# Optimization experiments

Hardware: AMD Instinct MI355X
Metric: run time of the kernel (lower is better)

## Reference

```python
import jax, jax.numpy as jnp
import numpy as np

NUM_HEADS = 8

def conv1x1(x, w, b):
    # x: [B,C,H,W], w: [O,C], b: [O]
    return jnp.einsum('bchw,oc->bohw', x, w) + b[None, :, None, None]

def setup_inputs() -> dict:
    key = jax.random.key(0)
    ks = jax.random.split(key, 8)
    B, C, H, W = 8, 256, 32, 32
    HF, WF = 128, 128
    s = 1.0 / np.sqrt(C)  # xavier-ish scale for 1x1 convs
    return {
        'x': jax.random.normal(ks[0], (B, C, H, W), jnp.float32),
        'featmap': jax.random.normal(ks[1], (B, C, HF, WF), jnp.float32),
        'wq': jax.random.normal(ks[2], (C, C), jnp.float32) * s,
        'bq': jnp.zeros((C,), jnp.float32),
        'wk': jax.random.normal(ks[3], (C, C), jnp.float32) * s,
        'bk': jnp.zeros((C,), jnp.float32),
        'wv': jax.random.normal(ks[4], (C, C), jnp.float32) * s,
        'bv': jnp.zeros((C,), jnp.float32),
        'wg': jax.random.normal(ks[5], (1, C), jnp.float32) * s,
        'bg': jnp.zeros((1,), jnp.float32),
    }

def _to_grid(t, h, w, rh, rw):
    # t: [B8, d, h*rh, w*rw] -> [B8, d, h, w, rh*rw] (aligned local grid per query pixel)
    b8, d = t.shape[:2]
    t = t.reshape(b8, d, h, rh, w, rw)
    return t.transpose(0, 1, 2, 4, 3, 5).reshape(b8, d, h, w, rh * rw)

def reference(x, featmap, wq, bq, wk, bk, wv, bv, wg, bg):
    B, C, H, W = x.shape
    HF, WF = featmap.shape[2:]
    head_dim = C // NUM_HEADS
    scaling = float(head_dim) ** -0.5
    rh, rw = HF // H, WF // W

    grid_weight = jax.nn.sigmoid(conv1x1(x, wg, bg))          # [B,1,H,W]
    q = conv1x1(x, wq, bq) * scaling                           # [B,C,H,W]
    k = conv1x1(featmap, wk, bk)                               # [B,C,HF,WF]
    v = conv1x1(featmap, wv, bv)

    q = q.reshape(B * NUM_HEADS, head_dim, H, W)
    k = k.reshape(B * NUM_HEADS, head_dim, HF, WF)
    v = v.reshape(B * NUM_HEADS, head_dim, HF, WF)

    k_grid = _to_grid(k, H, W, rh, rw)                         # [B8,d,H,W,P]
    v_grid = _to_grid(v, H, W, rh, rw)

    # ga_align_weight: correlate each query pixel with its aligned key grid
    attn = jnp.einsum('bchw,bchwp->bphw', q, k_grid)           # [B8,P,H,W]
    attn = jax.nn.softmax(attn, axis=1)
    # ga_align_map: weighted sum of aligned value grid
    out = jnp.einsum('bphw,bchwp->bchw', attn, v_grid)         # [B8,d,H,W]

    out = out.reshape(B, C, H, W) * grid_weight
    return out
```

## Files before the change

### kernel.cpp

```cpp
#include <hip/hip_runtime.h>

#define CDIM 256
#define SCALING 0.17677669529663687f

typedef _Float16 f16;
typedef f16 f16x4 __attribute__((ext_vector_type(4)));
typedef f16 f16x8 __attribute__((ext_vector_type(8)));
typedef float f32x4 __attribute__((ext_vector_type(4)));

#define MFMA(a, b, c) __builtin_amdgcn_mfma_f32_16x16x32_f16(a, b, c, 0, 0, 0)

__device__ __forceinline__ unsigned pack2(float a, float b) {
  union { f16 h[2]; unsigned u; } r;
  r.h[0] = (f16)a;
  r.h[1] = (f16)b;
  return r.u;
}

__global__ __launch_bounds__(256) void k_prep_w2(const float* __restrict__ wq,
                                                 const float* __restrict__ bq,
                                                 const float* __restrict__ wk,
                                                 const float* __restrict__ wv,
                                                 f16* __restrict__ W2h,
                                                 float* __restrict__ b2,
                                                 f16* __restrict__ wvh) {
  __shared__ float wk_s[32][8];
  const int t = threadIdx.x, ciO = blockIdx.x, hd = blockIdx.y;
  {
    int j = t >> 3, c8 = t & 7;
    wk_s[j][c8] = wk[(hd * 32 + j) * CDIM + ciO * 8 + c8];
    int idx = (hd * 32 + j) * CDIM + ciO * 8 + c8;
    wvh[idx] = (f16)wv[idx];
  }
  float wq_r[32];
#pragma unroll
  for (int j = 0; j < 32; ++j) wq_r[j] = wq[(hd * 32 + j) * CDIM + t];
  __syncthreads();
  for (int c8 = 0; c8 < 8; ++c8) {
    float acc = 0.f;
#pragma unroll
    for (int j = 0; j < 32; ++j) acc = fmaf(wq_r[j], wk_s[j][c8], acc);
    W2h[(size_t)(hd * CDIM + ciO * 8 + c8) * CDIM + t] = (f16)(acc * SCALING);
  }
  if (t < 8) {
    float a = 0.f;
    for (int j = 0; j < 32; ++j) a = fmaf(wk_s[j][t], bq[hd * 32 + j], a);
    b2[hd * CDIM + ciO * 8 + t] = a * SCALING;
  }
}

__global__ __launch_bounds__(256, 2) void k_qkw2(const float* __restrict__ x,
                                                 const f16* __restrict__ W2h,
                                                 const float* __restrict__ b2,
                                                 const float* __restrict__ wg,
                                                 const float* __restrict__ bg,
                                                 f16* __restrict__ qk,
                                                 float* __restrict__ gw, int b0) {
  __shared__ __align__(16) f16 A_l[256 * 40];
  __shared__ __align__(16) f16 B_l[64 * 40];
  const int t = threadIdx.x;
  const int p16 = blockIdx.x, hd = blockIdx.y, bz = blockIdx.z;
  const int bb = b0 + bz;
  const int lane = t & 63, wid = t >> 6, l15 = lane & 15, h4 = lane >> 4;
  f32x4 acc[4][4] = {};
  float gacc = 0.f;

  for (int kb = 0; kb < 8; ++kb) {
    __syncthreads();
#pragma unroll
    for (int it = 0; it < 4; ++it) {
      int e = it * 256 + t, ci = e >> 2, q = e & 3;
      *(f16x8*)(A_l + ci * 40 + q * 8) =
          *(const f16x8*)(W2h + (size_t)(hd * CDIM + ci) * CDIM + kb * 32 + q * 8);
    }
#pragma unroll
    for (int it = 0; it < 2; ++it) {
      int e = it * 256 + t, cx = e >> 4, p4 = e & 15;
      float4 v = *(const float4*)(x + (size_t)(bb * CDIM + kb * 32 + cx) * 1024 +
                                  p16 * 64 + p4 * 4);
      B_l[(p4 * 4 + 0) * 40 + cx] = (f16)v.x;
      B_l[(p4 * 4 + 1) * 40 + cx] = (f16)v.y;
      B_l[(p4 * 4 + 2) * 40 + cx] = (f16)v.z;
      B_l[(p4 * 4 + 3) * 40 + cx] = (f16)v.w;
    }
    __syncthreads();
    if (hd == 0 && wid == 3) {
#pragma unroll
      for (int cx = 0; cx < 32; ++cx)
        gacc = fmaf(wg[kb * 32 + cx], (float)B_l[lane * 40 + cx], gacc);
    }
    f16x8 a[4], bf[4];
#pragma unroll
    for (int mt = 0; mt < 4; ++mt)
      a[mt] = *(const f16x8*)(A_l + (wid * 64 + mt * 16 + l15) * 40 + h4 * 8);
#pragma unroll
    for (int nt = 0; nt < 4; ++nt)
      bf[nt] = *(const f16x8*)(B_l + (nt * 16 + l15) * 40 + h4 * 8);
#pragma unroll
    for (int mt = 0; mt < 4; ++mt)
#pragma unroll
      for (int nt = 0; nt < 4; ++nt) acc[mt][nt] = MFMA(a[mt], bf[nt], acc[mt][nt]);
  }
#pragma unroll
  for (int mt = 0; mt < 4; ++mt) {
    int ci0 = wid * 64 + mt * 16 + h4 * 4;
    float4 bvv = *(const float4*)(b2 + hd * CDIM + ci0);
#pragma unroll
    for (int nt = 0; nt < 4; ++nt) {
      int pix = p16 * 64 + nt * 16 + l15;
      union { f16 h[4]; unsigned long long u; } P;
      P.h[0] = (f16)(acc[mt][nt][0] + bvv.x);
      P.h[1] = (f16)(acc[mt][nt][1] + bvv.y);
      P.h[2] = (f16)(acc[mt][nt][2] + bvv.z);
      P.h[3] = (f16)(acc[mt][nt][3] + bvv.w);
      *(unsigned long long*)(qk + ((size_t)(bz * 1024 + pix) * 8 + hd) * CDIM + ci0) = P.u;
    }
  }
  if (hd == 0 && wid == 3)
    gw[bz * 1024 + p16 * 64 + lane] = 1.f / (1.f + __expf(-(gacc + bg[0])));
}

__global__ __launch_bounds__(256, 4) void k_attn(const float* __restrict__ feat,
                                                 const f16* __restrict__ qk,
                                                 f16* __restrict__ fa, int b0) {
  __shared__ __align__(16) f16 cip[4 * 4608];
  __shared__ __align__(16) f16 attn_l[4 * 512];
  const int t = threadIdx.x;
  const int h = blockIdx.x, w4 = blockIdx.y, bz = blockIdx.z;
  const int bb = b0 + bz;
  const int lane = t & 63, w = t >> 6, l15 = lane & 15, h4 = lane >> 4;
  const int pixb = h * 32 + w4 * 4;

  {
    f16x8 z = {};
    *(f16x8*)(attn_l + t * 8) = z;
  }
#pragma unroll
  for (int it = 0; it < 4; ++it) {
    int e = it * 256 + t, px = e >> 8, ci = e & 255;
    *(unsigned*)(cip + px * 4608 + ci * 18 + 16) = 0;
  }
  const float* fb = feat + (size_t)bb * (CDIM * 16384) + (h * 4) * 128 + w4 * 16;
#pragma unroll
  for (int it = 0; it < 16; ++it) {
    int e = it * 256 + t, px = e & 3, r = (e >> 2) & 3, ci = e >> 4;
    float4 v = *(const float4*)(fb + (size_t)ci * 16384 + r * 128 + px * 4);
    unsigned* d = (unsigned*)(cip + px * 4608 + ci * 18 + r * 4);
    d[0] = pack2(v.x, v.y);
    d[1] = pack2(v.z, v.w);
  }
  __syncthreads();

  const f16* qkg = qk + ((size_t)(bz * 1024 + pixb + w) * 8 + (l15 & 7)) * CDIM;
  const f16* cw = cip + w * 4608;
  f32x4 acc = {};
#pragma unroll
  for (int kb = 0; kb < 8; ++kb) {
    f16x8 a = *(const f16x8*)(qkg + kb * 32 + h4 * 8);
    f16x8 bf;
#pragma unroll
    for (int j = 0; j < 8; ++j) bf[j] = cw[(kb * 32 + h4 * 8 + j) * 18 + l15];
    acc = MFMA(a, bf, acc);
  }
  float at[4];
#pragma unroll
  for (int r = 0; r < 4; ++r) {
    float m = acc[r];
    m = fmaxf(m, __shfl_xor(m, 1, 64));
    m = fmaxf(m, __shfl_xor(m, 2, 64));
    m = fmaxf(m, __shfl_xor(m, 4, 64));
    m = fmaxf(m, __shfl_xor(m, 8, 64));
    float e = __expf(acc[r] - m);
    float s = e;
    s += __shfl_xor(s, 1, 64);
    s += __shfl_xor(s, 2, 64);
    s += __shfl_xor(s, 4, 64);
    s += __shfl_xor(s, 8, 64);
    at[r] = e / s;
  }
  if (h4 < 2) {
#pragma unroll
    for (int r = 0; r < 4; ++r) attn_l[w * 512 + l15 * 16 + h4 * 4 + r] = (f16)at[r];
  }
  f16x8 b5;
#pragma unroll
  for (int j = 0; j < 8; ++j) b5[j] = attn_l[w * 512 + (h4 * 8 + j) * 16 + l15];
  const f32x4 zero = {};
#pragma unroll
  for (int nt = 0; nt < 16; ++nt) {
    const unsigned* ap = (const unsigned*)(cw + (nt * 16 + l15) * 18 + h4 * 8);
    union { unsigned u[4]; f16x8 h; } A;
    A.u[0] = ap[0]; A.u[1] = ap[1]; A.u[2] = ap[2]; A.u[3] = ap[3];
    f32x4 d = MFMA(A.h, b5, zero);
    if (l15 < 8) {
      union { f16 h[4]; unsigned long long u; } P;
      P.h[0] = (f16)d[0]; P.h[1] = (f16)d[1]; P.h[2] = (f16)d[2]; P.h[3] = (f16)d[3];
      *(unsigned long long*)(fa + ((size_t)(bz * 8 + l15) * 1024 + pixb + w) * CDIM +
                             nt * 16 + h4 * 4) = P.u;
    }
  }
}

__global__ __launch_bounds__(256) void k_out(const f16* __restrict__ fa,
                                             const f16* __restrict__ wvh,
                                             const float* __restrict__ bv,
                                             const float* __restrict__ gw,
                                             float* __restrict__ out, int b0) {
  __shared__ __align__(16) f16 wv_l[32 * 264];
  __shared__ __align__(16) f16 fa_l[64 * 40];
  const int t = threadIdx.x;
  const int p16 = blockIdx.x, hd = blockIdx.y, bz = blockIdx.z;
  const int bb = b0 + bz;
  const int lane = t & 63, wid = t >> 6, l15 = lane & 15, h4 = lane >> 4;
#pragma unroll
  for (int it = 0; it < 4; ++it) {
    int e = it * 256 + t, c = e >> 5, ch = e & 31;
    *(f16x8*)(wv_l + c * 264 + ch * 8) =
        *(const f16x8*)(wvh + (size_t)(hd * 32 + c) * CDIM + ch * 8);
  }
  f32x4 acc[2] = {};
  for (int kb = 0; kb < 8; ++kb) {
    __syncthreads();
    {
      int pixl = t >> 2, q = t & 3;
      *(f16x8*)(fa_l + pixl * 40 + q * 8) =
          *(const f16x8*)(fa + ((size_t)(bz * 8 + hd) * 1024 + p16 * 64 + pixl) * CDIM +
                          kb * 32 + q * 8);
    }
    __syncthreads();
    f16x8 a = *(const f16x8*)(fa_l + (wid * 16 + l15) * 40 + h4 * 8);
#pragma unroll
    for (int nt = 0; nt < 2; ++nt) {
      f16x8 b = *(const f16x8*)(wv_l + (nt * 16 + l15) * 264 + kb * 32 + h4 * 8);
      acc[nt] = MFMA(a, b, acc[nt]);
    }
  }
  int pix0 = p16 * 64 + wid * 16 + h4 * 4;
  float4 g = *(const float4*)(gw + bz * 1024 + pix0);
#pragma unroll
  for (int nt = 0; nt < 2; ++nt) {
    int c = hd * 32 + nt * 16 + l15;
    float bvc = bv[c];
    float4 o;
    o.x = (acc[nt][0] + bvc) * g.x;
    o.y = (acc[nt][1] + bvc) * g.y;
    o.z = (acc[nt][2] + bvc) * g.z;
    o.w = (acc[nt][3] + bvc) * g.w;
    *(float4*)(out + (size_t)(bb * CDIM + c) * 1024 + pix0) = o;
  }
}

extern "C" void kernel_launch(void* const* d_in, const int* in_sizes, int n_in,
                              void* d_out, int out_size, void* d_ws, size_t ws_size,
                              hipStream_t stream) {
  const float* x = (const float*)d_in[0];
  const float* feat = (const float*)d_in[1];
  const float* wq = (const float*)d_in[2];
  const float* bq = (const float*)d_in[3];
  const float* wk = (const float*)d_in[4];
  const float* wv = (const float*)d_in[6];
  const float* bv = (const float*)d_in[7];
  const float* wg = (const float*)d_in[8];
  const float* bg = (const float*)d_in[9];
  float* out = (float*)d_out;

  char* ws = (char*)d_ws;
  f16* W2h = (f16*)ws;
  float* b2 = (float*)(ws + 1048576);
  f16* wvh = (f16*)(ws + 1056768);
  char* dyn = ws + 1187840;

  k_prep_w2<<<dim3(32, 8), 256, 0, stream>>>(wq, bq, wk, wv, W2h, b2, wvh);

  const size_t QK = 4194304, FA = 4194304, GW = 4096;
  if (ws_size >= 1187840 + 8 * (QK + FA + GW)) {
    f16* qkp = (f16*)dyn;
    f16* fap = (f16*)(dyn + 8 * QK);
    float* gwp = (float*)(dyn + 8 * (QK + FA));
    k_qkw2<<<dim3(16, 8, 8), 256, 0, stream>>>(x, W2h, b2, wg, bg, qkp, gwp, 0);
    k_attn<<<dim3(32, 8, 8), 256, 0, stream>>>(feat, qkp, fap, 0);
    k_out<<<dim3(16, 8, 8), 256, 0, stream>>>(fap, wvh, bv, gwp, out, 0);
  } else {
    f16* qkp = (f16*)dyn;
    f16* fap = (f16*)(dyn + QK);
    float* gwp = (float*)(dyn + QK + FA);
    for (int b = 0; b < 8; ++b) {
      k_qkw2<<<dim3(16, 8, 1), 256, 0, stream>>>(x, W2h, b2, wg, bg, qkp, gwp, b);
      k_attn<<<dim3(32, 8, 1), 256, 0, stream>>>(feat, qkp, fap, b);
      k_out<<<dim3(16, 8, 1), 256, 0, stream>>>(fap, wvh, bv, gwp, out, b);
    }
  }
}
```

Before: 80.35 us.

## Load MFMA operands directly from global and double-buffer the x tile

```diff
diff --git a/kernel.cpp b/kernel.cpp
--- a/kernel.cpp
+++ b/kernel.cpp
@@ -56,46 +56,47 @@
                                                  const float* __restrict__ bg,
                                                  f16* __restrict__ qk,
                                                  float* __restrict__ gw, int b0) {
-  __shared__ __align__(16) f16 A_l[256 * 40];
-  __shared__ __align__(16) f16 B_l[64 * 40];
+  __shared__ __align__(16) f16 B_l[2][64 * 40];
   const int t = threadIdx.x;
   const int p16 = blockIdx.x, hd = blockIdx.y, bz = blockIdx.z;
   const int bb = b0 + bz;
   const int lane = t & 63, wid = t >> 6, l15 = lane & 15, h4 = lane >> 4;
+  const f16* Whd = W2h + (size_t)hd * CDIM * CDIM;
   f32x4 acc[4][4] = {};
   float gacc = 0.f;
 
+  const int s_cx = t >> 4, s_p4 = t & 15;
+  const float* xs0 = x + (size_t)(bb * CDIM + s_cx) * 1024 + p16 * 64 + s_p4 * 4;
+#define STAGE_B(kb_, buf_)                                              \
+  {                                                                     \
+    float4 v0 = *(const float4*)(xs0 + (size_t)((kb_)*32) * 1024);      \
+    float4 v1 = *(const float4*)(xs0 + (size_t)((kb_)*32 + 16) * 1024); \
+    f16* d0 = &B_l[buf_][(s_p4 * 4) * 40 + s_cx];                       \
+    d0[0 * 40] = (f16)v0.x; d0[1 * 40] = (f16)v0.y;                     \
+    d0[2 * 40] = (f16)v0.z; d0[3 * 40] = (f16)v0.w;                     \
+    f16* d1 = d0 + 16;                                                  \
+    d1[0 * 40] = (f16)v1.x; d1[1 * 40] = (f16)v1.y;                     \
+    d1[2 * 40] = (f16)v1.z; d1[3 * 40] = (f16)v1.w;                     \
+  }
+
+  STAGE_B(0, 0);
   for (int kb = 0; kb < 8; ++kb) {
     __syncthreads();
-#pragma unroll
-    for (int it = 0; it < 4; ++it) {
-      int e = it * 256 + t, ci = e >> 2, q = e & 3;
-      *(f16x8*)(A_l + ci * 40 + q * 8) =
-          *(const f16x8*)(W2h + (size_t)(hd * CDIM + ci) * CDIM + kb * 32 + q * 8);
-    }
-#pragma unroll
-    for (int it = 0; it < 2; ++it) {
-      int e = it * 256 + t, cx = e >> 4, p4 = e & 15;
-      float4 v = *(const float4*)(x + (size_t)(bb * CDIM + kb * 32 + cx) * 1024 +
-                                  p16 * 64 + p4 * 4);
-      B_l[(p4 * 4 + 0) * 40 + cx] = (f16)v.x;
-      B_l[(p4 * 4 + 1) * 40 + cx] = (f16)v.y;
-      B_l[(p4 * 4 + 2) * 40 + cx] = (f16)v.z;
-      B_l[(p4 * 4 + 3) * 40 + cx] = (f16)v.w;
-    }
-    __syncthreads();
+    if (kb < 7) STAGE_B(kb + 1, (kb + 1) & 1);
+    const f16* Bcur = B_l[kb & 1];
     if (hd == 0 && wid == 3) {
 #pragma unroll
       for (int cx = 0; cx < 32; ++cx)
-        gacc = fmaf(wg[kb * 32 + cx], (float)B_l[lane * 40 + cx], gacc);
+        gacc = fmaf(wg[kb * 32 + cx], (float)Bcur[lane * 40 + cx], gacc);
     }
     f16x8 a[4], bf[4];
 #pragma unroll
     for (int mt = 0; mt < 4; ++mt)
-      a[mt] = *(const f16x8*)(A_l + (wid * 64 + mt * 16 + l15) * 40 + h4 * 8);
+      a[mt] = *(const f16x8*)(Whd + (size_t)(wid * 64 + mt * 16 + l15) * CDIM + kb * 32 +
+                              h4 * 8);
 #pragma unroll
     for (int nt = 0; nt < 4; ++nt)
-      bf[nt] = *(const f16x8*)(B_l + (nt * 16 + l15) * 40 + h4 * 8);
+      bf[nt] = *(const f16x8*)(Bcur + (nt * 16 + l15) * 40 + h4 * 8);
 #pragma unroll
     for (int mt = 0; mt < 4; ++mt)
 #pragma unroll
@@ -118,6 +119,7 @@
   }
   if (hd == 0 && wid == 3)
     gw[bz * 1024 + p16 * 64 + lane] = 1.f / (1.f + __expf(-(gacc + bg[0])));
+#undef STAGE_B
 }
 
 __global__ __launch_bounds__(256, 4) void k_attn(const float* __restrict__ feat,
@@ -207,7 +209,6 @@
                                              const float* __restrict__ gw,
                                              float* __restrict__ out, int b0) {
   __shared__ __align__(16) f16 wv_l[32 * 264];
-  __shared__ __align__(16) f16 fa_l[64 * 40];
   const int t = threadIdx.x;
   const int p16 = blockIdx.x, hd = blockIdx.y, bz = blockIdx.z;
   const int bb = b0 + bz;
@@ -218,17 +219,13 @@
     *(f16x8*)(wv_l + c * 264 + ch * 8) =
         *(const f16x8*)(wvh + (size_t)(hd * 32 + c) * CDIM + ch * 8);
   }
+  __syncthreads();
+  const f16* fap = fa + ((size_t)(bz * 8 + hd) * 1024 + p16 * 64 + wid * 16 + l15) * CDIM +
+                   h4 * 8;
   f32x4 acc[2] = {};
+#pragma unroll
   for (int kb = 0; kb < 8; ++kb) {
-    __syncthreads();
-    {
-      int pixl = t >> 2, q = t & 3;
-      *(f16x8*)(fa_l + pixl * 40 + q * 8) =
-          *(const f16x8*)(fa + ((size_t)(bz * 8 + hd) * 1024 + p16 * 64 + pixl) * CDIM +
-                          kb * 32 + q * 8);
-    }
-    __syncthreads();
-    f16x8 a = *(const f16x8*)(fa_l + (wid * 16 + l15) * 40 + h4 * 8);
+    f16x8 a = *(const f16x8*)(fap + kb * 32);
 #pragma unroll
     for (int nt = 0; nt < 2; ++nt) {
       f16x8 b = *(const f16x8*)(wv_l + (nt * 16 + l15) * 264 + kb * 32 + h4 * 8);
```

Measured after the change: 83.41 us. +3.8%, slower.
